# Kernel tuning notes

Hardware: AMD Instinct MI355X
Metric: run time of the kernel (lower is better)

## Reference

```python
import jax, jax.numpy as jnp
import numpy as np

HIDDEN_SIZE = 256
INPUT_SIZE = 4
N_CLASSES = 2


def setup_inputs() -> dict:
    key = jax.random.key(0)
    ks = jax.random.split(key, 12)
    B, T, H, I = 64, 2048, HIDDEN_SIZE, INPUT_SIZE
    s = 0.1
    return {
        "y": jax.random.normal(ks[0], (B, T), dtype=jnp.float32),
        "W_ih0": s * jax.random.normal(ks[1], (4 * H, I), dtype=jnp.float32),
        "W_hh0": s * jax.random.normal(ks[2], (4 * H, H), dtype=jnp.float32),
        "b_ih0": s * jax.random.normal(ks[3], (4 * H,), dtype=jnp.float32),
        "b_hh0": s * jax.random.normal(ks[4], (4 * H,), dtype=jnp.float32),
        "W_ih1": s * jax.random.normal(ks[5], (4 * H, H), dtype=jnp.float32),
        "W_hh1": s * jax.random.normal(ks[6], (4 * H, H), dtype=jnp.float32),
        "b_ih1": s * jax.random.normal(ks[7], (4 * H,), dtype=jnp.float32),
        "b_hh1": s * jax.random.normal(ks[8], (4 * H,), dtype=jnp.float32),
        "W_fc": s * jax.random.normal(ks[9], (N_CLASSES, H), dtype=jnp.float32),
        "b_fc": s * jax.random.normal(ks[10], (N_CLASSES,), dtype=jnp.float32),
    }


def _lstm_cell(x, h, c, Wi, Wh, bi, bh):
    # gate order i, f, g, o (torch convention, matches explicit slicing)
    gates = x @ Wi.T + bi + h @ Wh.T + bh  # [B, 4H]
    i, f, g, o = jnp.split(gates, 4, axis=-1)
    c_new = jax.nn.sigmoid(f) * c + jax.nn.sigmoid(i) * jnp.tanh(g)
    h_new = jax.nn.sigmoid(o) * jnp.tanh(c_new)
    return h_new, c_new


def reference(y, W_ih0, W_hh0, b_ih0, b_hh0, W_ih1, W_hh1, b_ih1, b_hh1, W_fc, b_fc):
    B, T = y.shape
    H = HIDDEN_SIZE
    # Sliding-window input: window [y[t-3], y[t-2], y[t-1], y[t]] with -100 pad
    padded = jnp.pad(y, ((0, 0), (0, INPUT_SIZE - 1)), constant_values=-100.0)
    seq = jnp.stack([jnp.roll(padded, s, axis=1) for s in range(INPUT_SIZE - 1, -1, -1)], axis=-1)
    seq = seq[:, :T]  # [B, T, 4]

    def step(carry, x_t):
        h0, c0, h1, c1 = carry
        h0, c0 = _lstm_cell(x_t, h0, c0, W_ih0, W_hh0, b_ih0, b_hh0)
        h1, c1 = _lstm_cell(h0, h1, c1, W_ih1, W_hh1, b_ih1, b_hh1)
        return (h0, c0, h1, c1), h1

    z = jnp.zeros((B, H), dtype=y.dtype)
    _, hs = jax.lax.scan(step, (z, z, z, z), jnp.swapaxes(seq, 0, 1))  # hs: [T, B, H]
    lstm_out = jnp.swapaxes(hs, 0, 1)  # [B, T, H]
    out = lstm_out @ W_fc.T + b_fc  # [B, T, N_CLASSES]
    return out
```

## Files before the change

### kernel.cpp

```cpp
#include <hip/hip_runtime.h>


#define NWG 32
#define BB 64
#define TT 2048
#define HH 256
#define HS 8
#define RS 32

#define WS_H0    0
#define WS_H1    16384
#define WS_FLAGS 32768
#define WS_CNT   33280
#define WS_WIN   33296
#define WS_NZERO 33296

typedef float  f32x4  __attribute__((ext_vector_type(4)));
typedef __bf16 bf16x8 __attribute__((ext_vector_type(8)));
typedef unsigned long long u64;
typedef unsigned int u32;

__device__ __forceinline__ float sigf(float x)   { return 1.0f / (1.0f + __expf(-x)); }
__device__ __forceinline__ float tanh_f(float x) { return 2.0f / (1.0f + __expf(-2.0f * x)) - 1.0f; }

__global__ void init_ws(u32* ws) {
  int i = blockIdx.x * blockDim.x + threadIdx.x;
  for (; i < WS_NZERO; i += gridDim.x * blockDim.x) ws[i] = 0u;
  if (blockIdx.x == 0 && threadIdx.x == 0) ((int*)ws)[WS_WIN] = -1;
}

__global__ __launch_bounds__(256, 1) void lstm2_persistent(
    const float* __restrict__ y,
    const float* __restrict__ Wih0, const float* __restrict__ Whh0,
    const float* __restrict__ bih0, const float* __restrict__ bhh0,
    const float* __restrict__ Wih1, const float* __restrict__ Whh1,
    const float* __restrict__ bih1, const float* __restrict__ bhh1,
    const float* __restrict__ Wfc,  const float* __restrict__ bfc,
    float* __restrict__ out,
    u32* __restrict__ ws)
{
  __bf16* h0buf = (__bf16*)(ws + WS_H0);
  __bf16* h1buf = (__bf16*)(ws + WS_H1);
  int*    flags = (int*)(ws + WS_FLAGS);
  int*    cnt   = (int*)(ws + WS_CNT);
  int*    winner= (int*)(ws + WS_WIN);

  const int tid  = threadIdx.x;

  __shared__ int s_w;
  if (tid == 0) {
    int xcc = __builtin_amdgcn_s_getreg(20 | (31 << 11)) & 0xF;
    int r = atomicAdd(&cnt[xcc], 1);
    if (r == NWG - 1) atomicCAS(winner, -1, xcc);
    int wv;
    while ((wv = __hip_atomic_load(winner, __ATOMIC_RELAXED,
                                   __HIP_MEMORY_SCOPE_AGENT)) == -1) {}
    s_w = (wv == xcc && r < NWG) ? r : -1;
  }
  __syncthreads();
  const int w = s_w;
  if (w < 0) return;

  const int wave = tid >> 6;
  const int lane = tid & 63;
  const int ml   = lane & 15;
  const int kq   = lane >> 4;

  __shared__ float lds_g0[RS][BB + 4];
  __shared__ float lds_g1[RS][BB + 4];
  __shared__ float s_wih0[RS][4];
  __shared__ float s_b0[RS];
  __shared__ float s_b1[RS];

  bf16x8 w0[2][8];
  bf16x8 w1[2][16];
  {
    #pragma unroll
    for (int n = 0; n < 2; n++) {
      const int r     = n * 16 + ml;
      const int d     = w * HS + (r & 7);
      const int rglob = (r >> 3) * 256 + d;
      #pragma unroll
      for (int s = 0; s < 8; s++) {
        const float* src = Whh0 + rglob * HH + s * 32 + kq * 8;
        bf16x8 f;
        #pragma unroll
        for (int j = 0; j < 8; j++) f[j] = (__bf16)src[j];
        w0[n][s] = f;
      }
      #pragma unroll
      for (int s = 0; s < 16; s++) {
        const int k = s * 32 + kq * 8;
        const float* src = (k < 256) ? (Wih1 + rglob * HH + k)
                                     : (Whh1 + rglob * HH + (k - 256));
        bf16x8 f;
        #pragma unroll
        for (int j = 0; j < 8; j++) f[j] = (__bf16)src[j];
        w1[n][s] = f;
      }
    }
  }

  if (tid < RS) {
    const int r     = tid;
    const int d     = w * HS + (r & 7);
    const int rglob = (r >> 3) * 256 + d;
    s_b0[r] = bih0[rglob] + bhh0[rglob];
    s_b1[r] = bih1[rglob] + bhh1[rglob];
    #pragma unroll
    for (int j = 0; j < 4; j++) s_wih0[r][j] = Wih0[rglob * 4 + j];
  }
  __syncthreads();

  float c0[2] = {0.f, 0.f};
  float c1[2] = {0.f, 0.f};

  const int b_epi = tid >> 2;
  const int dl    = (tid & 3) * 2;

  float x[4] = {-100.0f, -100.0f, -100.0f, -100.0f};

  for (int p = 0; p < TT + 2; p++) {
    const int par  = p & 1;
    const int parm = par ^ 1;

    const bool doL0 = (p < TT);
    const bool doL1 = (p >= 1 && p <= TT);

    bf16x8 a0[8], a1[8];
    {
      const int row = wave * 16 + ml;
      const __bf16* h0p = h0buf + (parm * NWG * BB + kq * BB + row) * HS;
      const __bf16* h1p = h1buf + (par  * NWG * BB + kq * BB + row) * HS;
      #pragma unroll
      for (int s = 0; s < 8; s++)
        asm volatile("global_load_dwordx4 %0, %1, off sc0"
                     : "=v"(a0[s]) : "v"(h0p + s * 4 * BB * HS) : "memory");
      #pragma unroll
      for (int s = 0; s < 8; s++)
        asm volatile("global_load_dwordx4 %0, %1, off sc0"
                     : "=v"(a1[s]) : "v"(h1p + s * 4 * BB * HS) : "memory");
    }

    x[0] = x[1]; x[1] = x[2]; x[2] = x[3];
    x[3] = (p < TT) ? y[b_epi * TT + p] : -100.0f;

    asm volatile("s_waitcnt vmcnt(0)" ::: "memory");
    __builtin_amdgcn_sched_barrier(0);

    f32x4 acc00 = {0.f,0.f,0.f,0.f}, acc01 = {0.f,0.f,0.f,0.f};
    f32x4 acc10 = {0.f,0.f,0.f,0.f}, acc11 = {0.f,0.f,0.f,0.f};

    if (doL0) {
      #pragma unroll
      for (int s = 0; s < 8; s++) {
        acc00 = __builtin_amdgcn_mfma_f32_16x16x32_bf16(a0[s], w0[0][s], acc00, 0, 0, 0);
        acc01 = __builtin_amdgcn_mfma_f32_16x16x32_bf16(a0[s], w0[1][s], acc01, 0, 0, 0);
      }
    }
    if (doL1) {
      #pragma unroll
      for (int s = 0; s < 8; s++) {
        acc10 = __builtin_amdgcn_mfma_f32_16x16x32_bf16(a0[s], w1[0][s], acc10, 0, 0, 0);
        acc11 = __builtin_amdgcn_mfma_f32_16x16x32_bf16(a0[s], w1[1][s], acc11, 0, 0, 0);
      }
      #pragma unroll
      for (int s = 0; s < 8; s++) {
        acc10 = __builtin_amdgcn_mfma_f32_16x16x32_bf16(a1[s], w1[0][s + 8], acc10, 0, 0, 0);
        acc11 = __builtin_amdgcn_mfma_f32_16x16x32_bf16(a1[s], w1[1][s + 8], acc11, 0, 0, 0);
      }
    }

    {
      const int bb = wave * 16 + kq * 4;
      if (doL0) {
        #pragma unroll
        for (int j = 0; j < 4; j++) lds_g0[ml     ][bb + j] = acc00[j];
        #pragma unroll
        for (int j = 0; j < 4; j++) lds_g0[16 + ml][bb + j] = acc01[j];
      }
      if (doL1) {
        #pragma unroll
        for (int j = 0; j < 4; j++) lds_g1[ml     ][bb + j] = acc10[j];
        #pragma unroll
        for (int j = 0; j < 4; j++) lds_g1[16 + ml][bb + j] = acc11[j];
      }
    }
    __syncthreads();

    if (doL0) {
      float hn[2];
      #pragma unroll
      for (int e = 0; e < 2; e++) {
        const int d = dl + e;
        const float gi = lds_g0[d     ][b_epi] + s_b0[d     ]
          + s_wih0[d     ][0]*x[0] + s_wih0[d     ][1]*x[1] + s_wih0[d     ][2]*x[2] + s_wih0[d     ][3]*x[3];
        const float gf = lds_g0[8 + d ][b_epi] + s_b0[8 + d ]
          + s_wih0[8 + d ][0]*x[0] + s_wih0[8 + d ][1]*x[1] + s_wih0[8 + d ][2]*x[2] + s_wih0[8 + d ][3]*x[3];
        const float gg = lds_g0[16 + d][b_epi] + s_b0[16 + d]
          + s_wih0[16 + d][0]*x[0] + s_wih0[16 + d][1]*x[1] + s_wih0[16 + d][2]*x[2] + s_wih0[16 + d][3]*x[3];
        const float go = lds_g0[24 + d][b_epi] + s_b0[24 + d]
          + s_wih0[24 + d][0]*x[0] + s_wih0[24 + d][1]*x[1] + s_wih0[24 + d][2]*x[2] + s_wih0[24 + d][3]*x[3];
        const float cn = sigf(gf) * c0[e] + sigf(gi) * tanh_f(gg);
        c0[e] = cn;
        hn[e] = sigf(go) * tanh_f(cn);
      }
      union { __bf16 h[2]; u32 u; } pk;
      pk.h[0] = (__bf16)hn[0]; pk.h[1] = (__bf16)hn[1];
      *(u32*)(h0buf + (par * NWG * BB + w * BB + b_epi) * HS + dl) = pk.u;
    }

    if (doL1) {
      float hn[2];
      #pragma unroll
      for (int e = 0; e < 2; e++) {
        const int d = dl + e;
        const float gi = lds_g1[d     ][b_epi] + s_b1[d     ];
        const float gf = lds_g1[8 + d ][b_epi] + s_b1[8 + d ];
        const float gg = lds_g1[16 + d][b_epi] + s_b1[16 + d];
        const float go = lds_g1[24 + d][b_epi] + s_b1[24 + d];
        const float cn = sigf(gf) * c1[e] + sigf(gi) * tanh_f(gg);
        c1[e] = cn;
        hn[e] = sigf(go) * tanh_f(cn);
      }
      union { __bf16 h[2]; u32 u; } pk;
      pk.h[0] = (__bf16)hn[0]; pk.h[1] = (__bf16)hn[1];
      *(u32*)(h1buf + (parm * NWG * BB + w * BB + b_epi) * HS + dl) = pk.u;
    }

    asm volatile("s_waitcnt vmcnt(0)" ::: "memory");
    __syncthreads();
    if (tid == 0)
      __hip_atomic_store(&flags[w * 16], p + 2, __ATOMIC_RELAXED,
                         __HIP_MEMORY_SCOPE_WORKGROUP);

    if (p >= 2) {
      const int t = p - 2;
      const int b = 2 * w + (wave & 1);
      const int c = wave >> 1;
      const __bf16* h1r = h1buf + (par * NWG * BB + (lane >> 1) * BB + b) * HS + (lane & 1) * 4;
      union { u64 u; __bf16 h[4]; } c4;
      c4.u = __hip_atomic_load((u64*)h1r, __ATOMIC_RELAXED,
                               __HIP_MEMORY_SCOPE_AGENT);
      float s = 0.f;
      #pragma unroll
      for (int j = 0; j < 4; j++)
        s += (float)c4.h[j] * Wfc[c * HH + lane * 4 + j];
      #pragma unroll
      for (int off = 32; off > 0; off >>= 1) s += __shfl_down(s, off, 64);
      if (lane == 0) out[b * (TT * 2) + t * 2 + c] = s + bfc[c];
    }

    if (tid < NWG) {
      while (__hip_atomic_load(&flags[tid * 16], __ATOMIC_RELAXED,
                               __HIP_MEMORY_SCOPE_AGENT) < p + 2) {}
    }
    __syncthreads();
  }
}

extern "C" void kernel_launch(void* const* d_in, const int* in_sizes, int n_in,
                              void* d_out, int out_size, void* d_ws, size_t ws_size,
                              hipStream_t stream) {
  u32* ws = (u32*)d_ws;
  init_ws<<<dim3(64), dim3(256), 0, stream>>>(ws);
  lstm2_persistent<<<dim3(256), dim3(256), 0, stream>>>(
      (const float*)d_in[0],  (const float*)d_in[1], (const float*)d_in[2],
      (const float*)d_in[3],  (const float*)d_in[4], (const float*)d_in[5],
      (const float*)d_in[6],  (const float*)d_in[7], (const float*)d_in[8],
      (const float*)d_in[9],  (const float*)d_in[10],
      (float*)d_out, ws);
}
```

Baseline: 6.323 ms.

## Split recurrent work across 64 workgroups with 4 hidden units each

Each persistent workgroup now owns 4 hidden units (16 gate rows) instead of 8. This doubles the workgroup count to 64, halves each block's MFMA and weight-register load per timestep, and lifts the launch bounds to 2 blocks per CU. Two workgroups now write halves of the same 8-wide bf16 hidden strip, using scalar bf16 stores. The layer-1 input and recurrent products go into separate accumulators to shorten the dependency chain. The cost is a grid-wide flag barrier over twice as many workgroups every step, and the FC epilogue now runs on two waves per block.

```diff
diff --git a/kernel.cpp b/kernel.cpp
--- a/kernel.cpp
+++ b/kernel.cpp
@@ -1,19 +1,21 @@
 #include <hip/hip_runtime.h>
 
 
-#define NWG 32
+#define NWG 64
+#define NSTRIP 32
 #define BB 64
 #define TT 2048
 #define HH 256
 #define HS 8
-#define RS 32
+#define HSW 4
+#define RS 16
 
 #define WS_H0    0
 #define WS_H1    16384
 #define WS_FLAGS 32768
-#define WS_CNT   33280
-#define WS_WIN   33296
-#define WS_NZERO 33296
+#define WS_CNT   33792
+#define WS_WIN   33808
+#define WS_NZERO 33808
 
 typedef float  f32x4  __attribute__((ext_vector_type(4)));
 typedef __bf16 bf16x8 __attribute__((ext_vector_type(8)));
@@ -29,7 +31,7 @@
   if (blockIdx.x == 0 && threadIdx.x == 0) ((int*)ws)[WS_WIN] = -1;
 }
 
-__global__ __launch_bounds__(256, 1) void lstm2_persistent(
+__global__ __launch_bounds__(256, 2) void lstm2_persistent(
     const float* __restrict__ y,
     const float* __restrict__ Wih0, const float* __restrict__ Whh0,
     const float* __restrict__ bih0, const float* __restrict__ bhh0,
@@ -72,39 +74,34 @@
   __shared__ float s_b0[RS];
   __shared__ float s_b1[RS];
 
-  bf16x8 w0[2][8];
-  bf16x8 w1[2][16];
+  bf16x8 w0f[8];
+  bf16x8 w1f[16];
   {
+    const int r     = ml;
+    const int rglob = (r >> 2) * 256 + w * HSW + (r & 3);
     #pragma unroll
-    for (int n = 0; n < 2; n++) {
-      const int r     = n * 16 + ml;
-      const int d     = w * HS + (r & 7);
-      const int rglob = (r >> 3) * 256 + d;
-      #pragma unroll
-      for (int s = 0; s < 8; s++) {
-        const float* src = Whh0 + rglob * HH + s * 32 + kq * 8;
-        bf16x8 f;
-        #pragma unroll
-        for (int j = 0; j < 8; j++) f[j] = (__bf16)src[j];
-        w0[n][s] = f;
-      }
-      #pragma unroll
-      for (int s = 0; s < 16; s++) {
-        const int k = s * 32 + kq * 8;
-        const float* src = (k < 256) ? (Wih1 + rglob * HH + k)
-                                     : (Whh1 + rglob * HH + (k - 256));
-        bf16x8 f;
-        #pragma unroll
-        for (int j = 0; j < 8; j++) f[j] = (__bf16)src[j];
-        w1[n][s] = f;
-      }
+    for (int s = 0; s < 8; s++) {
+      const float* src = Whh0 + rglob * HH + s * 32 + kq * 8;
+      bf16x8 f;
+      #pragma unroll
+      for (int j = 0; j < 8; j++) f[j] = (__bf16)src[j];
+      w0f[s] = f;
+    }
+    #pragma unroll
+    for (int s = 0; s < 16; s++) {
+      const int k = s * 32 + kq * 8;
+      const float* src = (k < 256) ? (Wih1 + rglob * HH + k)
+                                   : (Whh1 + rglob * HH + (k - 256));
+      bf16x8 f;
+      #pragma unroll
+      for (int j = 0; j < 8; j++) f[j] = (__bf16)src[j];
+      w1f[s] = f;
     }
   }
 
   if (tid < RS) {
     const int r     = tid;
-    const int d     = w * HS + (r & 7);
-    const int rglob = (r >> 3) * 256 + d;
+    const int rglob = (r >> 2) * 256 + w * HSW + (r & 3);
     s_b0[r] = bih0[rglob] + bhh0[rglob];
     s_b1[r] = bih1[rglob] + bhh1[rglob];
     #pragma unroll
@@ -112,11 +109,10 @@
   }
   __syncthreads();
 
-  float c0[2] = {0.f, 0.f};
-  float c1[2] = {0.f, 0.f};
+  float c0 = 0.f, c1 = 0.f;
 
   const int b_epi = tid >> 2;
-  const int dl    = (tid & 3) * 2;
+  const int dl    = tid & 3;
 
   float x[4] = {-100.0f, -100.0f, -100.0f, -100.0f};
 
@@ -130,8 +126,8 @@
     bf16x8 a0[8], a1[8];
     {
       const int row = wave * 16 + ml;
-      const __bf16* h0p = h0buf + (parm * NWG * BB + kq * BB + row) * HS;
-      const __bf16* h1p = h1buf + (par  * NWG * BB + kq * BB + row) * HS;
+      const __bf16* h0p = h0buf + (parm * NSTRIP * BB + kq * BB + row) * HS;
+      const __bf16* h1p = h1buf + (par  * NSTRIP * BB + kq * BB + row) * HS;
       #pragma unroll
       for (int s = 0; s < 8; s++)
         asm volatile("global_load_dwordx4 %0, %1, off sc0"
@@ -148,84 +144,61 @@
     asm volatile("s_waitcnt vmcnt(0)" ::: "memory");
     __builtin_amdgcn_sched_barrier(0);
 
-    f32x4 acc00 = {0.f,0.f,0.f,0.f}, acc01 = {0.f,0.f,0.f,0.f};
-    f32x4 acc10 = {0.f,0.f,0.f,0.f}, acc11 = {0.f,0.f,0.f,0.f};
+    f32x4 acc0  = {0.f,0.f,0.f,0.f};
+    f32x4 acc1a = {0.f,0.f,0.f,0.f};
+    f32x4 acc1b = {0.f,0.f,0.f,0.f};
 
     if (doL0) {
       #pragma unroll
-      for (int s = 0; s < 8; s++) {
-        acc00 = __builtin_amdgcn_mfma_f32_16x16x32_bf16(a0[s], w0[0][s], acc00, 0, 0, 0);
-        acc01 = __builtin_amdgcn_mfma_f32_16x16x32_bf16(a0[s], w0[1][s], acc01, 0, 0, 0);
-      }
+      for (int s = 0; s < 8; s++)
+        acc0 = __builtin_amdgcn_mfma_f32_16x16x32_bf16(a0[s], w0f[s], acc0, 0, 0, 0);
     }
     if (doL1) {
       #pragma unroll
-      for (int s = 0; s < 8; s++) {
-        acc10 = __builtin_amdgcn_mfma_f32_16x16x32_bf16(a0[s], w1[0][s], acc10, 0, 0, 0);
-        acc11 = __builtin_amdgcn_mfma_f32_16x16x32_bf16(a0[s], w1[1][s], acc11, 0, 0, 0);
-      }
-      #pragma unroll
-      for (int s = 0; s < 8; s++) {
-        acc10 = __builtin_amdgcn_mfma_f32_16x16x32_bf16(a1[s], w1[0][s + 8], acc10, 0, 0, 0);
-        acc11 = __builtin_amdgcn_mfma_f32_16x16x32_bf16(a1[s], w1[1][s + 8], acc11, 0, 0, 0);
-      }
+      for (int s = 0; s < 8; s++)
+        acc1a = __builtin_amdgcn_mfma_f32_16x16x32_bf16(a0[s], w1f[s], acc1a, 0, 0, 0);
+      #pragma unroll
+      for (int s = 0; s < 8; s++)
+        acc1b = __builtin_amdgcn_mfma_f32_16x16x32_bf16(a1[s], w1f[s + 8], acc1b, 0, 0, 0);
     }
 
     {
       const int bb = wave * 16 + kq * 4;
       if (doL0) {
         #pragma unroll
-        for (int j = 0; j < 4; j++) lds_g0[ml     ][bb + j] = acc00[j];
-        #pragma unroll
-        for (int j = 0; j < 4; j++) lds_g0[16 + ml][bb + j] = acc01[j];
+        for (int j = 0; j < 4; j++) lds_g0[ml][bb + j] = acc0[j];
       }
       if (doL1) {
         #pragma unroll
-        for (int j = 0; j < 4; j++) lds_g1[ml     ][bb + j] = acc10[j];
-        #pragma unroll
-        for (int j = 0; j < 4; j++) lds_g1[16 + ml][bb + j] = acc11[j];
+        for (int j = 0; j < 4; j++) lds_g1[ml][bb + j] = acc1a[j] + acc1b[j];
       }
     }
     __syncthreads();
 
     if (doL0) {
-      float hn[2];
-      #pragma unroll
-      for (int e = 0; e < 2; e++) {
-        const int d = dl + e;
-        const float gi = lds_g0[d     ][b_epi] + s_b0[d     ]
-          + s_wih0[d     ][0]*x[0] + s_wih0[d     ][1]*x[1] + s_wih0[d     ][2]*x[2] + s_wih0[d     ][3]*x[3];
-        const float gf = lds_g0[8 + d ][b_epi] + s_b0[8 + d ]
-          + s_wih0[8 + d ][0]*x[0] + s_wih0[8 + d ][1]*x[1] + s_wih0[8 + d ][2]*x[2] + s_wih0[8 + d ][3]*x[3];
-        const float gg = lds_g0[16 + d][b_epi] + s_b0[16 + d]
-          + s_wih0[16 + d][0]*x[0] + s_wih0[16 + d][1]*x[1] + s_wih0[16 + d][2]*x[2] + s_wih0[16 + d][3]*x[3];
-        const float go = lds_g0[24 + d][b_epi] + s_b0[24 + d]
-          + s_wih0[24 + d][0]*x[0] + s_wih0[24 + d][1]*x[1] + s_wih0[24 + d][2]*x[2] + s_wih0[24 + d][3]*x[3];
-        const float cn = sigf(gf) * c0[e] + sigf(gi) * tanh_f(gg);
-        c0[e] = cn;
-        hn[e] = sigf(go) * tanh_f(cn);
-      }
-      union { __bf16 h[2]; u32 u; } pk;
-      pk.h[0] = (__bf16)hn[0]; pk.h[1] = (__bf16)hn[1];
-      *(u32*)(h0buf + (par * NWG * BB + w * BB + b_epi) * HS + dl) = pk.u;
+      const float gi = lds_g0[dl     ][b_epi] + s_b0[dl     ]
+        + s_wih0[dl     ][0]*x[0] + s_wih0[dl     ][1]*x[1] + s_wih0[dl     ][2]*x[2] + s_wih0[dl     ][3]*x[3];
+      const float gf = lds_g0[4 + dl ][b_epi] + s_b0[4 + dl ]
+        + s_wih0[4 + dl ][0]*x[0] + s_wih0[4 + dl ][1]*x[1] + s_wih0[4 + dl ][2]*x[2] + s_wih0[4 + dl ][3]*x[3];
+      const float gg = lds_g0[8 + dl ][b_epi] + s_b0[8 + dl ]
+        + s_wih0[8 + dl ][0]*x[0] + s_wih0[8 + dl ][1]*x[1] + s_wih0[8 + dl ][2]*x[2] + s_wih0[8 + dl ][3]*x[3];
+      const float go = lds_g0[12 + dl][b_epi] + s_b0[12 + dl]
+        + s_wih0[12 + dl][0]*x[0] + s_wih0[12 + dl][1]*x[1] + s_wih0[12 + dl][2]*x[2] + s_wih0[12 + dl][3]*x[3];
+      const float cn = sigf(gf) * c0 + sigf(gi) * tanh_f(gg);
+      c0 = cn;
+      const float hn = sigf(go) * tanh_f(cn);
+      h0buf[(par * NSTRIP * BB + (w >> 1) * BB + b_epi) * HS + (w & 1) * 4 + dl] = (__bf16)hn;
     }
 
     if (doL1) {
-      float hn[2];
-      #pragma unroll
-      for (int e = 0; e < 2; e++) {
-        const int d = dl + e;
-        const float gi = lds_g1[d     ][b_epi] + s_b1[d     ];
-        const float gf = lds_g1[8 + d ][b_epi] + s_b1[8 + d ];
-        const float gg = lds_g1[16 + d][b_epi] + s_b1[16 + d];
-        const float go = lds_g1[24 + d][b_epi] + s_b1[24 + d];
-        const float cn = sigf(gf) * c1[e] + sigf(gi) * tanh_f(gg);
-        c1[e] = cn;
-        hn[e] = sigf(go) * tanh_f(cn);
-      }
-      union { __bf16 h[2]; u32 u; } pk;
-      pk.h[0] = (__bf16)hn[0]; pk.h[1] = (__bf16)hn[1];
-      *(u32*)(h1buf + (parm * NWG * BB + w * BB + b_epi) * HS + dl) = pk.u;
+      const float gi = lds_g1[dl     ][b_epi] + s_b1[dl     ];
+      const float gf = lds_g1[4 + dl ][b_epi] + s_b1[4 + dl ];
+      const float gg = lds_g1[8 + dl ][b_epi] + s_b1[8 + dl ];
+      const float go = lds_g1[12 + dl][b_epi] + s_b1[12 + dl];
+      const float cn = sigf(gf) * c1 + sigf(gi) * tanh_f(gg);
+      c1 = cn;
+      const float hn = sigf(go) * tanh_f(cn);
+      h1buf[(parm * NSTRIP * BB + (w >> 1) * BB + b_epi) * HS + (w & 1) * 4 + dl] = (__bf16)hn;
     }
 
     asm volatile("s_waitcnt vmcnt(0)" ::: "memory");
@@ -234,11 +207,11 @@
       __hip_atomic_store(&flags[w * 16], p + 2, __ATOMIC_RELAXED,
                          __HIP_MEMORY_SCOPE_WORKGROUP);
 
-    if (p >= 2) {
+    if (p >= 2 && wave < 2) {
       const int t = p - 2;
-      const int b = 2 * w + (wave & 1);
-      const int c = wave >> 1;
-      const __bf16* h1r = h1buf + (par * NWG * BB + (lane >> 1) * BB + b) * HS + (lane & 1) * 4;
+      const int b = w;
+      const int c = wave;
+      const __bf16* h1r = h1buf + (par * NSTRIP * BB + (lane >> 1) * BB + b) * HS + (lane & 1) * 4;
       union { u64 u; __bf16 h[4]; } c4;
       c4.u = __hip_atomic_load((u64*)h1r, __ATOMIC_RELAXED,
                                __HIP_MEMORY_SCOPE_AGENT);
@@ -264,7 +237,7 @@
                               hipStream_t stream) {
   u32* ws = (u32*)d_ws;
   init_ws<<<dim3(64), dim3(256), 0, stream>>>(ws);
-  lstm2_persistent<<<dim3(256), dim3(256), 0, stream>>>(
+  lstm2_persistent<<<dim3(768), dim3(256), 0, stream>>>(
       (const float*)d_in[0],  (const float*)d_in[1], (const float*)d_in[2],
       (const float*)d_in[3],  (const float*)d_in[4], (const float*)d_in[5],
       (const float*)d_in[6],  (const float*)d_in[7], (const float*)d_in[8],
```

Result: faster. 5.927 ms (-6.3%).
